# Kernel optimization log

Hardware: AMD Instinct MI355X
Metric: run time of the kernel (lower is better)

## Reference

```python
import jax, jax.numpy as jnp
import numpy as np

SHARPNESS = 2.0
WRITE_RATE_TARGET = 1.0 / 2000.0
EPS = 1e-12  # F.normalize default eps

B, L, S, D = 8, 512, 128, 256


def _l2norm(x):
    # matches F.normalize(p=2): x / max(||x||, eps)
    n = jnp.sqrt(jnp.sum(x * x, axis=-1, keepdims=True))
    return x / jnp.maximum(n, EPS)


def setup_inputs() -> dict:
    key = jax.random.key(0)
    ks = jax.random.split(key, 6)
    s = 0.05
    return {
        "init_memory": jnp.zeros((B, S, D), jnp.float32),
        "hidden_seq": jax.random.normal(ks[0], (B, L, D), jnp.float32),
        "masks": jnp.ones((B, L, 1), jnp.float32),
        "Wq": jax.random.normal(ks[1], (D, D), jnp.float32) * s,
        "bq": jnp.zeros((D,), jnp.float32),
        "Wk": jax.random.normal(ks[2], (D, D), jnp.float32) * s,
        "bk": jnp.zeros((D,), jnp.float32),
        "Wv": jax.random.normal(ks[3], (D, D), jnp.float32) * s,
        "bv": jnp.zeros((D,), jnp.float32),
        "Wg": jax.random.normal(ks[4], (1, D), jnp.float32) * s,
        "bg": jnp.zeros((1,), jnp.float32),
    }


def reference(init_memory, hidden_seq, masks, Wq, bq, Wk, bk, Wv, bv, Wg, bg):
    def step(mem, xs):
        h, m = xs  # h: (B, D), m: (B, 1)
        mem_n = _l2norm(mem)  # (B, S, D)
        # --- read ---
        q = h @ Wq.T + bq
        q_n = _l2norm(q)
        sim = jnp.einsum("bsd,bd->bs", mem_n, q_n)
        read_w = jax.nn.softmax(sim * SHARPNESS, axis=-1)
        read_v = jnp.einsum("bs,bsd->bd", read_w, mem)
        # --- write ---
        wk = h @ Wk.T + bk
        wv = h @ Wv.T + bv
        gate = jax.nn.sigmoid(h @ Wg.T + bg)  # (B, 1), soft gate
        wk_n = _l2norm(wk)
        wsim = jnp.einsum("bsd,bd->bs", mem_n, wk_n)
        write_w = jax.nn.softmax(wsim * SHARPNESS, axis=-1)
        write_op = gate[:, None, :] * write_w[:, :, None]  # (B, S, 1)
        next_mem = mem + write_op * (wv[:, None, :] - mem)
        next_mem = next_mem * m[:, :, None]  # mask reset, (B,1,1) broadcast
        sp = (jnp.mean(gate) - WRITE_RATE_TARGET) ** 2
        return next_mem, (read_v, sp)

    xs = (jnp.swapaxes(hidden_seq, 0, 1), jnp.swapaxes(masks, 0, 1))  # (L, B, ...)
    _, (reads, sps) = jax.lax.scan(step, init_memory, xs)
    read_seq = jnp.swapaxes(reads, 0, 1)  # (B, L, D)
    return read_seq, jnp.mean(sps)
```

## Files before the change

kernel.cpp:

```cpp
#include <hip/hip_runtime.h>
#include <math.h>

#define NB 8
#define NL 512
#define NS 128
#define ND 256

constexpr float SHARPNESS = 2.0f;
constexpr float WTGT = 1.0f / 2000.0f;
constexpr float EPS = 1e-12f;

__global__ __launch_bounds__(256) void proj_kernel(
    const float* __restrict__ hseq,
    const float* __restrict__ Wq, const float* __restrict__ bq,
    const float* __restrict__ Wk, const float* __restrict__ bk,
    const float* __restrict__ Wv, const float* __restrict__ bv,
    const float* __restrict__ Wg, const float* __restrict__ bg,
    float* __restrict__ Qo, float* __restrict__ Ko,
    float* __restrict__ Vo, float* __restrict__ Go)
{
    __shared__ float hs[16][ND + 4];
    const int tid = threadIdx.x;
    const int bl0 = blockIdx.x * 16;

    for (int k = 0; k < 16; ++k)
        hs[k][tid] = hseq[(size_t)(bl0 + k) * ND + tid];
    __syncthreads();

    const int d = tid;
    for (int mat = 0; mat < 3; ++mat) {
        const float* W    = (mat == 0) ? Wq : (mat == 1) ? Wk : Wv;
        const float* bias = (mat == 0) ? bq : (mat == 1) ? bk : bv;
        float* O          = (mat == 0) ? Qo : (mat == 1) ? Ko : Vo;
        float acc[16];
        const float b0 = bias[d];
        #pragma unroll
        for (int i = 0; i < 16; ++i) acc[i] = b0;
        const float4* Wrow = (const float4*)(W + (size_t)d * ND);
        for (int j4 = 0; j4 < 64; ++j4) {
            const float4 w4 = Wrow[j4];
            #pragma unroll
            for (int i = 0; i < 16; ++i) {
                const float4 h4 = *(const float4*)&hs[i][j4 * 4];
                acc[i] = fmaf(w4.x, h4.x,
                         fmaf(w4.y, h4.y,
                         fmaf(w4.z, h4.z,
                         fmaf(w4.w, h4.w, acc[i]))));
            }
        }
        #pragma unroll
        for (int i = 0; i < 16; ++i)
            O[(size_t)(bl0 + i) * ND + d] = acc[i];
    }

    {
        const int i = tid >> 4, j0 = (tid & 15) * 16;
        float p = 0.f;
        #pragma unroll
        for (int j = 0; j < 16; ++j)
            p = fmaf(Wg[j0 + j], hs[i][j0 + j], p);
        #pragma unroll
        for (int m = 1; m < 16; m <<= 1) p += __shfl_xor(p, m);
        if ((tid & 15) == 0) {
            const float z = p + bg[0];
            Go[bl0 + i] = 1.f / (1.f + __expf(-z));
        }
    }
}

__global__ __launch_bounds__(64) void norm_kernel(
    const float* __restrict__ Qb, const float* __restrict__ Kb,
    float* __restrict__ Qn2, float* __restrict__ Kn2)
{
    const int bl = blockIdx.x;
    const int lane = threadIdx.x;
    const float4 q4 = ((const float4*)(Qb + (size_t)bl * ND))[lane];
    const float4 k4 = ((const float4*)(Kb + (size_t)bl * ND))[lane];
    float qq = q4.x*q4.x + q4.y*q4.y + q4.z*q4.z + q4.w*q4.w;
    float kk = k4.x*k4.x + k4.y*k4.y + k4.z*k4.z + k4.w*k4.w;
    #pragma unroll
    for (int m = 1; m < 64; m <<= 1) { qq += __shfl_xor(qq, m); kk += __shfl_xor(kk, m); }
    if (lane == 0) { Qn2[bl] = qq; Kn2[bl] = kk; }
}

__global__ __launch_bounds__(256) void sp_kernel(
    const float* __restrict__ Go, float* __restrict__ out_sp)
{
    const int tid = threadIdx.x;
    float s = 0.f;
    for (int l = tid; l < NL; l += 256) {
        float gsum = 0.f;
        #pragma unroll
        for (int b = 0; b < NB; ++b) gsum += Go[b * NL + l];
        const float d = gsum * (1.f / NB) - WTGT;
        s += d * d;
    }
    #pragma unroll
    for (int m = 1; m < 64; m <<= 1) s += __shfl_xor(s, m);
    __shared__ float ws[4];
    if ((tid & 63) == 0) ws[tid >> 6] = s;
    __syncthreads();
    if (tid == 0) out_sp[0] = (ws[0] + ws[1] + ws[2] + ws[3]) * (1.f / NL);
}

__global__ __launch_bounds__(512, 2) void scan_kernel(
    const float* __restrict__ init_mem, const float* __restrict__ masks,
    const float* __restrict__ Qb, const float* __restrict__ Kb,
    const float* __restrict__ Vb, const float* __restrict__ Gb,
    const float* __restrict__ Qn2, const float* __restrict__ Kn2,
    float* __restrict__ out)
{
    const int b    = blockIdx.x;
    const int t    = (int)threadIdx.x;
    const int lane = t & 63;
    const int w    = t >> 6;
    const int r    = t >> 2;
    const int c    = t & 3;
    const int d0   = c * 64;

    __shared__ float redmax[2][8];
    __shared__ float redsum[2][8];
    __shared__ float rvpart[8][ND];

    float mem[64];
    {
        const float4* p4 = (const float4*)(init_mem + ((size_t)b * NS + r) * ND + d0);
        #pragma unroll
        for (int j4 = 0; j4 < 16; ++j4) {
            const float4 v = p4[j4];
            mem[4*j4+0] = v.x; mem[4*j4+1] = v.y; mem[4*j4+2] = v.z; mem[4*j4+3] = v.w;
        }
    }

    float qv[64], kv[64];
    {
        const float4* qp = (const float4*)(Qb + ((size_t)b * NL) * ND + d0);
        const float4* kp = (const float4*)(Kb + ((size_t)b * NL) * ND + d0);
        #pragma unroll
        for (int j4 = 0; j4 < 16; ++j4) {
            const float4 a_ = qp[j4];
            qv[4*j4+0] = a_.x; qv[4*j4+1] = a_.y; qv[4*j4+2] = a_.z; qv[4*j4+3] = a_.w;
            const float4 b_ = kp[j4];
            kv[4*j4+0] = b_.x; kv[4*j4+1] = b_.y; kv[4*j4+2] = b_.z; kv[4*j4+3] = b_.w;
        }
    }

    const bool h1 = (lane & 4)  != 0;
    const bool h2 = (lane & 8)  != 0;
    const bool h3 = (lane & 16) != 0;
    const bool h4 = (lane & 32) != 0;
    const int off = (h1 ? 32 : 0) + (h2 ? 16 : 0) + (h3 ? 8 : 0) + (h4 ? 4 : 0);

    for (int step = 0; step < NL; ++step) {
        const size_t blt = (size_t)b * NL + step;
        const float qn2  = Qn2[blt];
        const float kn2  = Kn2[blt];
        const float g    = Gb[blt];
        const float mval = masks[blt];

        float dq = 0.f, dk = 0.f, nn = 0.f;
        #pragma unroll
        for (int j = 0; j < 64; ++j) {
            const float m_ = mem[j];
            dq = fmaf(m_, qv[j], dq);
            dk = fmaf(m_, kv[j], dk);
            nn = fmaf(m_, m_, nn);
        }

        {
            const float4* qp = (const float4*)(Qb + (blt + 1) * ND + d0);
            const float4* kp = (const float4*)(Kb + (blt + 1) * ND + d0);
            #pragma unroll
            for (int j4 = 0; j4 < 16; ++j4) {
                const float4 a_ = qp[j4];
                qv[4*j4+0] = a_.x; qv[4*j4+1] = a_.y; qv[4*j4+2] = a_.z; qv[4*j4+3] = a_.w;
                const float4 b_ = kp[j4];
                kv[4*j4+0] = b_.x; kv[4*j4+1] = b_.y; kv[4*j4+2] = b_.z; kv[4*j4+3] = b_.w;
            }
        }

        dq += __shfl_xor(dq, 1); dq += __shfl_xor(dq, 2);
        dk += __shfl_xor(dk, 1); dk += __shfl_xor(dk, 2);
        nn += __shfl_xor(nn, 1); nn += __shfl_xor(nn, 2);

        const float rinv = 1.f / fmaxf(sqrtf(nn),  EPS);
        const float qni  = 1.f / fmaxf(sqrtf(qn2), EPS);
        const float kni  = 1.f / fmaxf(sqrtf(kn2), EPS);
        const float sim  = dq * rinv * qni * SHARPNESS;
        const float wsim = dk * rinv * kni * SHARPNESS;

        float mx1 = sim, mx2 = wsim;
        #pragma unroll
        for (int m_ = 1; m_ < 64; m_ <<= 1) {
            mx1 = fmaxf(mx1, __shfl_xor(mx1, m_));
            mx2 = fmaxf(mx2, __shfl_xor(mx2, m_));
        }
        if (lane == 0) { redmax[0][w] = mx1; redmax[1][w] = mx2; }
        __syncthreads();
        float M1 = redmax[0][0], M2 = redmax[1][0];
        #pragma unroll
        for (int i = 1; i < 8; ++i) {
            M1 = fmaxf(M1, redmax[0][i]);
            M2 = fmaxf(M2, redmax[1][i]);
        }
        const float e1 = __expf(sim  - M1);
        const float e2 = __expf(wsim - M2);
        float s1 = e1, s2 = e2;
        #pragma unroll
        for (int m_ = 1; m_ < 64; m_ <<= 1) {
            s1 += __shfl_xor(s1, m_);
            s2 += __shfl_xor(s2, m_);
        }
        if (lane == 0) { redsum[0][w] = s1; redsum[1][w] = s2; }
        __syncthreads();
        float S1 = 0.f, S2 = 0.f;
        #pragma unroll
        for (int i = 0; i < 8; ++i) { S1 += redsum[0][i]; S2 += redsum[1][i]; }
        const float rw = e1 * (4.f / S1);
        const float a  = g * (e2 * (4.f / S2));

        float red[32];
        #pragma unroll
        for (int k2 = 0; k2 < 32; ++k2) {
            const float plo = rw * mem[k2];
            const float phi = rw * mem[32 + k2];
            red[k2] = (h1 ? phi : plo) + __shfl_xor(h1 ? plo : phi, 4);
        }
        #pragma unroll
        for (int k2 = 0; k2 < 16; ++k2)
            red[k2] = (h2 ? red[16+k2] : red[k2]) + __shfl_xor(h2 ? red[k2] : red[16+k2], 8);
        #pragma unroll
        for (int k2 = 0; k2 < 8; ++k2)
            red[k2] = (h3 ? red[8+k2] : red[k2]) + __shfl_xor(h3 ? red[k2] : red[8+k2], 16);
        #pragma unroll
        for (int k2 = 0; k2 < 4; ++k2)
            red[k2] = (h4 ? red[4+k2] : red[k2]) + __shfl_xor(h4 ? red[k2] : red[4+k2], 32);
        *(float4*)&rvpart[w][d0 + off] = make_float4(red[0], red[1], red[2], red[3]);

        {
            const float4* vp = (const float4*)(Vb + blt * ND + d0);
            #pragma unroll
            for (int j4 = 0; j4 < 16; ++j4) {
                const float4 v4 = vp[j4];
                mem[4*j4+0] = fmaf(a, v4.x - mem[4*j4+0], mem[4*j4+0]);
                mem[4*j4+1] = fmaf(a, v4.y - mem[4*j4+1], mem[4*j4+1]);
                mem[4*j4+2] = fmaf(a, v4.z - mem[4*j4+2], mem[4*j4+2]);
                mem[4*j4+3] = fmaf(a, v4.w - mem[4*j4+3], mem[4*j4+3]);
            }
        }
        if (mval != 1.0f) {
            #pragma unroll
            for (int j = 0; j < 64; ++j) mem[j] *= mval;
        }

        __syncthreads();
        if (t < ND) {
            float s = 0.f;
            #pragma unroll
            for (int ww2 = 0; ww2 < 8; ++ww2) s += rvpart[ww2][t];
            out[blt * ND + t] = s;
        }
    }
}

extern "C" void kernel_launch(void* const* d_in, const int* in_sizes, int n_in,
                              void* d_out, int out_size, void* d_ws, size_t ws_size,
                              hipStream_t stream)
{
    (void)in_sizes; (void)n_in; (void)out_size; (void)ws_size;

    const float* init_mem = (const float*)d_in[0];
    const float* hseq     = (const float*)d_in[1];
    const float* masks    = (const float*)d_in[2];
    const float* Wq = (const float*)d_in[3];  const float* bq = (const float*)d_in[4];
    const float* Wk = (const float*)d_in[5];  const float* bk = (const float*)d_in[6];
    const float* Wv = (const float*)d_in[7];  const float* bv = (const float*)d_in[8];
    const float* Wg = (const float*)d_in[9];  const float* bg = (const float*)d_in[10];
    float* out = (float*)d_out;

    float* ws  = (float*)d_ws;
    float* Qb  = ws;
    float* Kb  = Qb + (size_t)NB * NL * ND;
    float* Vb  = Kb + (size_t)NB * NL * ND;
    float* Gb  = Vb + (size_t)NB * NL * ND;
    float* Qn2 = Gb + NB * NL;
    float* Kn2 = Qn2 + NB * NL;

    proj_kernel<<<(NB * NL) / 16, 256, 0, stream>>>(hseq, Wq, bq, Wk, bk, Wv, bv,
                                                    Wg, bg, Qb, Kb, Vb, Gb);
    norm_kernel<<<NB * NL, 64, 0, stream>>>(Qb, Kb, Qn2, Kn2);
    sp_kernel<<<1, 256, 0, stream>>>(Gb, out + (size_t)NB * NL * ND);
    scan_kernel<<<NB, 512, 0, stream>>>(init_mem, masks, Qb, Kb, Vb, Gb, Qn2, Kn2, out);
}
```

Before: 6.876 ms.

## Drop softmax max-reduction using bounded cosine logits and restructure scan loads

Because both logits are cosine similarities scaled by 2, they are bounded in [-2,2], so the softmax max pass and its block barrier are removed and exp is applied directly. The per-step inverse norms of q and k are moved into the norm kernel. The q/k prefetch registers are dropped in favour of loading q and k inside the dot loop, and v is loaded early into registers. Launch bounds are relaxed to one block per CU to give more registers. This saves one __syncthreads and a cross-wave reduction per step. The trade-off is that q/k load latency is now exposed each step instead of being prefetched.

```diff
diff --git a/kernel.cpp b/kernel.cpp
--- a/kernel.cpp
+++ b/kernel.cpp
@@ -70,7 +70,7 @@
 
 __global__ __launch_bounds__(64) void norm_kernel(
     const float* __restrict__ Qb, const float* __restrict__ Kb,
-    float* __restrict__ Qn2, float* __restrict__ Kn2)
+    float* __restrict__ Qni, float* __restrict__ Kni)
 {
     const int bl = blockIdx.x;
     const int lane = threadIdx.x;
@@ -80,7 +80,10 @@
     float kk = k4.x*k4.x + k4.y*k4.y + k4.z*k4.z + k4.w*k4.w;
     #pragma unroll
     for (int m = 1; m < 64; m <<= 1) { qq += __shfl_xor(qq, m); kk += __shfl_xor(kk, m); }
-    if (lane == 0) { Qn2[bl] = qq; Kn2[bl] = kk; }
+    if (lane == 0) {
+        Qni[bl] = 1.f / fmaxf(sqrtf(qq), EPS);
+        Kni[bl] = 1.f / fmaxf(sqrtf(kk), EPS);
+    }
 }
 
 __global__ __launch_bounds__(256) void sp_kernel(
@@ -103,11 +106,11 @@
     if (tid == 0) out_sp[0] = (ws[0] + ws[1] + ws[2] + ws[3]) * (1.f / NL);
 }
 
-__global__ __launch_bounds__(512, 2) void scan_kernel(
+__global__ __launch_bounds__(512, 1) void scan_kernel(
     const float* __restrict__ init_mem, const float* __restrict__ masks,
     const float* __restrict__ Qb, const float* __restrict__ Kb,
     const float* __restrict__ Vb, const float* __restrict__ Gb,
-    const float* __restrict__ Qn2, const float* __restrict__ Kn2,
+    const float* __restrict__ Qni, const float* __restrict__ Kni,
     float* __restrict__ out)
 {
     const int b    = blockIdx.x;
@@ -118,30 +121,16 @@
     const int c    = t & 3;
     const int d0   = c * 64;
 
-    __shared__ float redmax[2][8];
-    __shared__ float redsum[2][8];
-    __shared__ float rvpart[8][ND];
+    __shared__ float2 redsum[8];
+    __shared__ float  rvpart[8][ND];
 
     float mem[64];
     {
         const float4* p4 = (const float4*)(init_mem + ((size_t)b * NS + r) * ND + d0);
         #pragma unroll
-        for (int j4 = 0; j4 < 16; ++j4) {
-            const float4 v = p4[j4];
-            mem[4*j4+0] = v.x; mem[4*j4+1] = v.y; mem[4*j4+2] = v.z; mem[4*j4+3] = v.w;
-        }
-    }
-
-    float qv[64], kv[64];
-    {
-        const float4* qp = (const float4*)(Qb + ((size_t)b * NL) * ND + d0);
-        const float4* kp = (const float4*)(Kb + ((size_t)b * NL) * ND + d0);
-        #pragma unroll
-        for (int j4 = 0; j4 < 16; ++j4) {
-            const float4 a_ = qp[j4];
-            qv[4*j4+0] = a_.x; qv[4*j4+1] = a_.y; qv[4*j4+2] = a_.z; qv[4*j4+3] = a_.w;
-            const float4 b_ = kp[j4];
-            kv[4*j4+0] = b_.x; kv[4*j4+1] = b_.y; kv[4*j4+2] = b_.z; kv[4*j4+3] = b_.w;
+        for (int j = 0; j < 16; ++j) {
+            const float4 v = p4[j];
+            mem[4*j+0] = v.x; mem[4*j+1] = v.y; mem[4*j+2] = v.z; mem[4*j+3] = v.w;
         }
     }
 
@@ -151,31 +140,38 @@
     const bool h4 = (lane & 32) != 0;
     const int off = (h1 ? 32 : 0) + (h2 ? 16 : 0) + (h3 ? 8 : 0) + (h4 ? 4 : 0);
 
+    #pragma unroll 1
     for (int step = 0; step < NL; ++step) {
         const size_t blt = (size_t)b * NL + step;
-        const float qn2  = Qn2[blt];
-        const float kn2  = Kn2[blt];
-        const float g    = Gb[blt];
+        const float qni  = Qni[blt];
+        const float kni  = Kni[blt];
+        const float g_   = Gb[blt];
         const float mval = masks[blt];
 
         float dq = 0.f, dk = 0.f, nn = 0.f;
-        #pragma unroll
-        for (int j = 0; j < 64; ++j) {
-            const float m_ = mem[j];
-            dq = fmaf(m_, qv[j], dq);
-            dk = fmaf(m_, kv[j], dk);
-            nn = fmaf(m_, m_, nn);
-        }
-
         {
-            const float4* qp = (const float4*)(Qb + (blt + 1) * ND + d0);
-            const float4* kp = (const float4*)(Kb + (blt + 1) * ND + d0);
-            #pragma unroll
-            for (int j4 = 0; j4 < 16; ++j4) {
-                const float4 a_ = qp[j4];
-                qv[4*j4+0] = a_.x; qv[4*j4+1] = a_.y; qv[4*j4+2] = a_.z; qv[4*j4+3] = a_.w;
-                const float4 b_ = kp[j4];
-                kv[4*j4+0] = b_.x; kv[4*j4+1] = b_.y; kv[4*j4+2] = b_.z; kv[4*j4+3] = b_.w;
+            const float4* qp = (const float4*)(Qb + blt * ND + d0);
+            const float4* kp = (const float4*)(Kb + blt * ND + d0);
+            #pragma unroll
+            for (int j = 0; j < 16; ++j) {
+                const float4 q4 = qp[j];
+                const float4 k4 = kp[j];
+                const float m0 = mem[4*j+0], m1 = mem[4*j+1];
+                const float m2 = mem[4*j+2], m3 = mem[4*j+3];
+                dq = fmaf(m0, q4.x, fmaf(m1, q4.y, fmaf(m2, q4.z, fmaf(m3, q4.w, dq))));
+                dk = fmaf(m0, k4.x, fmaf(m1, k4.y, fmaf(m2, k4.z, fmaf(m3, k4.w, dk))));
+                nn = fmaf(m0, m0, fmaf(m1, m1, fmaf(m2, m2, fmaf(m3, m3, nn))));
+            }
+        }
+
+        float v4r[64];
+        {
+            const float4* vp = (const float4*)(Vb + blt * ND + d0);
+            #pragma unroll
+            for (int j = 0; j < 16; ++j) {
+                const float4 v4 = vp[j];
+                v4r[4*j+0] = v4.x; v4r[4*j+1] = v4.y;
+                v4r[4*j+2] = v4.z; v4r[4*j+3] = v4.w;
             }
         }
 
@@ -183,41 +179,26 @@
         dk += __shfl_xor(dk, 1); dk += __shfl_xor(dk, 2);
         nn += __shfl_xor(nn, 1); nn += __shfl_xor(nn, 2);
 
-        const float rinv = 1.f / fmaxf(sqrtf(nn),  EPS);
-        const float qni  = 1.f / fmaxf(sqrtf(qn2), EPS);
-        const float kni  = 1.f / fmaxf(sqrtf(kn2), EPS);
+        const float rinv = 1.f / fmaxf(sqrtf(nn), EPS);
         const float sim  = dq * rinv * qni * SHARPNESS;
         const float wsim = dk * rinv * kni * SHARPNESS;
-
-        float mx1 = sim, mx2 = wsim;
-        #pragma unroll
-        for (int m_ = 1; m_ < 64; m_ <<= 1) {
-            mx1 = fmaxf(mx1, __shfl_xor(mx1, m_));
-            mx2 = fmaxf(mx2, __shfl_xor(mx2, m_));
-        }
-        if (lane == 0) { redmax[0][w] = mx1; redmax[1][w] = mx2; }
-        __syncthreads();
-        float M1 = redmax[0][0], M2 = redmax[1][0];
-        #pragma unroll
-        for (int i = 1; i < 8; ++i) {
-            M1 = fmaxf(M1, redmax[0][i]);
-            M2 = fmaxf(M2, redmax[1][i]);
-        }
-        const float e1 = __expf(sim  - M1);
-        const float e2 = __expf(wsim - M2);
+        const float e1 = __expf(sim);
+        const float e2 = __expf(wsim);
+
         float s1 = e1, s2 = e2;
         #pragma unroll
         for (int m_ = 1; m_ < 64; m_ <<= 1) {
             s1 += __shfl_xor(s1, m_);
             s2 += __shfl_xor(s2, m_);
         }
-        if (lane == 0) { redsum[0][w] = s1; redsum[1][w] = s2; }
+        if (lane == 0) redsum[w] = make_float2(s1, s2);
         __syncthreads();
         float S1 = 0.f, S2 = 0.f;
         #pragma unroll
-        for (int i = 0; i < 8; ++i) { S1 += redsum[0][i]; S2 += redsum[1][i]; }
+        for (int i = 0; i < 8; ++i) { const float2 sv = redsum[i]; S1 += sv.x; S2 += sv.y; }
+
         const float rw = e1 * (4.f / S1);
-        const float a  = g * (e2 * (4.f / S2));
+        const float a  = g_ * (e2 * (4.f / S2));
 
         float red[32];
         #pragma unroll
@@ -237,17 +218,9 @@
             red[k2] = (h4 ? red[4+k2] : red[k2]) + __shfl_xor(h4 ? red[k2] : red[4+k2], 32);
         *(float4*)&rvpart[w][d0 + off] = make_float4(red[0], red[1], red[2], red[3]);
 
-        {
-            const float4* vp = (const float4*)(Vb + blt * ND + d0);
-            #pragma unroll
-            for (int j4 = 0; j4 < 16; ++j4) {
-                const float4 v4 = vp[j4];
-                mem[4*j4+0] = fmaf(a, v4.x - mem[4*j4+0], mem[4*j4+0]);
-                mem[4*j4+1] = fmaf(a, v4.y - mem[4*j4+1], mem[4*j4+1]);
-                mem[4*j4+2] = fmaf(a, v4.z - mem[4*j4+2], mem[4*j4+2]);
-                mem[4*j4+3] = fmaf(a, v4.w - mem[4*j4+3], mem[4*j4+3]);
-            }
-        }
+        #pragma unroll
+        for (int j = 0; j < 64; ++j)
+            mem[j] = fmaf(a, v4r[j] - mem[j], mem[j]);
         if (mval != 1.0f) {
             #pragma unroll
             for (int j = 0; j < 64; ++j) mem[j] *= mval;
@@ -257,7 +230,7 @@
         if (t < ND) {
             float s = 0.f;
             #pragma unroll
-            for (int ww2 = 0; ww2 < 8; ++ww2) s += rvpart[ww2][t];
+            for (int ww = 0; ww < 8; ++ww) s += rvpart[ww][t];
             out[blt * ND + t] = s;
         }
     }
@@ -283,12 +256,12 @@
     float* Kb  = Qb + (size_t)NB * NL * ND;
     float* Vb  = Kb + (size_t)NB * NL * ND;
     float* Gb  = Vb + (size_t)NB * NL * ND;
-    float* Qn2 = Gb + NB * NL;
-    float* Kn2 = Qn2 + NB * NL;
+    float* Qni = Gb + NB * NL;
+    float* Kni = Qni + NB * NL;
 
     proj_kernel<<<(NB * NL) / 16, 256, 0, stream>>>(hseq, Wq, bq, Wk, bk, Wv, bv,
                                                     Wg, bg, Qb, Kb, Vb, Gb);
-    norm_kernel<<<NB * NL, 64, 0, stream>>>(Qb, Kb, Qn2, Kn2);
+    norm_kernel<<<NB * NL, 64, 0, stream>>>(Qb, Kb, Qni, Kni);
     sp_kernel<<<1, 256, 0, stream>>>(Gb, out + (size_t)NB * NL * ND);
-    scan_kernel<<<NB, 512, 0, stream>>>(init_mem, masks, Qb, Kb, Vb, Gb, Qn2, Kn2, out);
-}
+    scan_kernel<<<NB, 512, 0, stream>>>(init_mem, masks, Qb, Kb, Vb, Gb, Qni, Kni, out);
+}
```

Result: faster. 6.076 ms (-11.6%).
